# Performance work log

Measured on AMD Instinct MI355X. Metric: run time of the kernel, lower is better.

The kernel has to match this reference:

```python
import jax, jax.numpy as jnp
from jax import lax
import numpy as np

STRIDE = 1
PADDING = 1
DILATION = 1


def setup_inputs() -> dict:
    key = jax.random.key(0)
    k1, k2, k3, k4 = jax.random.split(key, 4)
    B, Cin, Cout, H, W, K, G = 32, 256, 256, 56, 56, 3, 8
    x = jax.random.normal(k1, (B, Cin, H, W), dtype=jnp.float32)
    conv = jax.random.normal(k2, (Cout, Cin, K, K), dtype=jnp.float32)
    S = jax.random.normal(k3, (Cin, G), dtype=jnp.float32)
    T = jax.random.normal(k4, (Cout, G), dtype=jnp.float32)
    return {"x": x, "conv": conv, "S": S, "T": T}


def reference(x, conv, S, T):
    # Faithful to FLGC.forward (training path).
    Cin = S.shape[0]
    Cout = T.shape[0]
    s_hat = jax.nn.softmax(S, axis=1)            # [Cin, G]
    t_hat = jax.nn.softmax(T, axis=1)            # [Cout, G]
    s = jnp.argmax(s_hat, axis=1)                # group id per input channel
    t = jnp.argmax(t_hat, axis=1)                # group id per output filter
    # Input channel c is scaled by s_hat[c, s[c]] inside its group.
    x_sc = x * s_hat[jnp.arange(Cin), s][None, :, None, None]
    # Filter o uses weight conv[o,c] * t_hat[o, t[o]] only where s[c] == t[o];
    # masking weights to zero elsewhere makes one dense conv equal the per-group convs.
    gate = (s[None, :] == t[:, None]).astype(conv.dtype)          # [Cout, Cin]
    w = conv * t_hat[jnp.arange(Cout), t][:, None, None, None] * gate[:, :, None, None]
    out_full = lax.conv_general_dilated(
        x_sc, w,
        window_strides=(STRIDE, STRIDE),
        padding=[(PADDING, PADDING), (PADDING, PADDING)],
        rhs_dilation=(DILATION, DILATION),
    )  # [B, Cout, H', W'], channel o = group-conv output of filter o
    # Original concatenates group outputs (channels ordered by perm = stable sort of t),
    # then indexes that with perm again: final[:, j] = out_full[:, perm[perm[j]]].
    perm = jnp.argsort(t * Cout + jnp.arange(Cout))  # stable group-major order
    return out_full[:, perm[perm]]
```

## Files before the change

kernel.cpp:

```cpp
#include <hip/hip_runtime.h>

#define M_SI    0
#define M_SO    256
#define M_CLIST 512
#define M_FLIST 768
#define M_DEST  1024
#define M_CBASE 1280
#define M_FBASE 1288
#define M_CCNT  1296
#define M_FCNT  1304
#define M_WOFFE 1312
#define WPACK_BYTE_OFF 16384
#define XR_BYTE_OFF   (4u << 20)
#define SLOT_ELEMS    3444736ull
#define SLOT_BYTES    (SLOT_ELEMS * 2ull)

typedef short bf16x8 __attribute__((ext_vector_type(8)));
typedef float f32x4  __attribute__((ext_vector_type(4)));

__device__ __forceinline__ unsigned short f2bf(float f) {
    unsigned u = __float_as_uint(f);
    u += 0x7fffu + ((u >> 16) & 1u);
    return (unsigned short)(u >> 16);
}

__device__ __forceinline__ void gl_lds16(const void* g, void* l) {
    __builtin_amdgcn_global_load_lds((const __attribute__((address_space(1))) unsigned int*)g,
                                     (__attribute__((address_space(3))) unsigned int*)l, 16, 0, 0);
}

__global__ __launch_bounds__(256) void flgc_setup(const float* __restrict__ S,
                                                  const float* __restrict__ T,
                                                  int* __restrict__ meta) {
    __shared__ float si[256], so[256];
    __shared__ int gin[256], gout[256];
    __shared__ int cnt_in[8], cnt_out[8], cb[8], fb[8];
    __shared__ int perm[256], destl[256];
    const int c = threadIdx.x;

    {
        float m = S[c * 8]; int am = 0;
        for (int k = 1; k < 8; ++k) { float v = S[c * 8 + k]; if (v > m) { m = v; am = k; } }
        float s = 0.f;
        for (int k = 0; k < 8; ++k) s += expf(S[c * 8 + k] - m);
        si[c] = 1.0f / s; gin[c] = am;
    }
    {
        float m = T[c * 8]; int am = 0;
        for (int k = 1; k < 8; ++k) { float v = T[c * 8 + k]; if (v > m) { m = v; am = k; } }
        float s = 0.f;
        for (int k = 0; k < 8; ++k) s += expf(T[c * 8 + k] - m);
        so[c] = 1.0f / s; gout[c] = am;
    }
    __syncthreads();
    const int g = gin[c], go = gout[c];
    int r1 = 0, r2 = 0;
    for (int i = 0; i < c; ++i) { r1 += (gin[i] == g); r2 += (gout[i] == go); }
    if (c < 8) {
        int n1 = 0, n2 = 0;
        for (int i = 0; i < 256; ++i) { n1 += (gin[i] == c); n2 += (gout[i] == c); }
        cnt_in[c] = n1; cnt_out[c] = n2;
    }
    __syncthreads();
    if (c == 0) {
        int a = 0, b = 0;
        for (int k = 0; k < 8; ++k) { cb[k] = a; a += cnt_in[k]; fb[k] = b; b += cnt_out[k]; }
    }
    __syncthreads();
    meta[M_CLIST + cb[g] + r1] = c;
    perm[fb[go] + r2] = c;
    __syncthreads();
    const int ppc = perm[perm[c]];
    destl[ppc] = c;
    __syncthreads();
    ((float*)meta)[M_SI + c] = si[c];
    ((float*)meta)[M_SO + c] = so[c];
    meta[M_FLIST + c] = perm[c];
    meta[M_DEST + c]  = destl[c];
    if (c < 8) {
        meta[M_CBASE + c] = cb[c];
        meta[M_FBASE + c] = fb[c];
        meta[M_CCNT + c]  = cnt_in[c];
        meta[M_FCNT + c]  = cnt_out[c];
    }
    if (c == 0) {
        int a = 0;
        for (int k = 0; k < 8; ++k) {
            meta[M_WOFFE + k] = a;
            const int nq  = (cnt_in[k] + 31) >> 5;
            const int mfa = (cnt_out[k] + 15) >> 4;
            a += nq * mfa * 9 * 512;
        }
        meta[M_WOFFE + 8] = a;
    }
}

__global__ void flgc_pack(const float* __restrict__ conv, const int* __restrict__ meta,
                          unsigned short* __restrict__ wpack) {
    const float* si = (const float*)meta + M_SI;
    const float* so = (const float*)meta + M_SO;
    const int total = meta[M_WOFFE + 8];
    for (int idx = blockIdx.x * blockDim.x + threadIdx.x; idx < total;
         idx += gridDim.x * blockDim.x) {
        int gg = 0;
        while (gg < 7 && idx >= meta[M_WOFFE + gg + 1]) ++gg;
        const int local = idx - meta[M_WOFFE + gg];
        const int fcnt = meta[M_FCNT + gg], ccnt = meta[M_CCNT + gg];
        const int mfall = (fcnt + 15) >> 4;
        const int fragidx = local >> 9, e = local & 511;
        const int lane = e >> 3, j = e & 7;
        const int tap = fragidx % 9, t2 = fragidx / 9;
        const int mf = t2 % mfall, q = t2 / mfall;
        const int fl = mf * 16 + (lane & 15);
        const int cl = q * 32 + (lane >> 4) * 8 + j;
        float v = 0.f;
        if (fl < fcnt && cl < ccnt) {
            const int F  = meta[M_FLIST + meta[M_FBASE + gg] + fl];
            const int CH = meta[M_CLIST + meta[M_CBASE + gg] + cl];
            v = conv[(F * 256 + CH) * 9 + tap] * si[CH] * so[F];
        }
        wpack[idx] = f2bf(v);
    }
}

__global__ __launch_bounds__(256) void flgc_reorder(const float* __restrict__ x,
                                                    const int* __restrict__ meta,
                                                    unsigned short* __restrict__ xr) {
    __shared__ float lds[32][65];
    const int r = blockIdx.x;
    const int b = blockIdx.y;
    const int slot = blockIdx.z;
    const int g = slot >> 1, q = slot & 1;
    const int ccnt = meta[M_CCNT + g];
    int nq = (ccnt + 31) >> 5; if (nq > 2) nq = 2;
    if (q >= nq) return;
    const int cbas = meta[M_CBASE + g];
    const int row = r - 1;
    const int colx = threadIdx.x & 63;
    const int cl0 = threadIdx.x >> 6;
    const int ic = colx - 1;
    const bool ok = ((unsigned)row < 56u) && ((unsigned)ic < 56u);

    int chn[8];
#pragma unroll
    for (int i = 0; i < 8; ++i) {
        const int cgl = q * 32 + cl0 + i * 4;
        chn[i] = (cgl < ccnt) ? meta[M_CLIST + cbas + cgl] : -1;
    }
    const float* xb = x + (size_t)b * 256 * 3136 + row * 56 + ic;
    float v[8];
#pragma unroll
    for (int i = 0; i < 8; ++i) v[i] = 0.f;
#pragma unroll
    for (int i = 0; i < 8; ++i)
        if (ok && chn[i] >= 0) v[i] = xb[(size_t)chn[i] * 3136];
#pragma unroll
    for (int i = 0; i < 8; ++i) lds[cl0 + i * 4][colx] = v[i];
    __syncthreads();

    unsigned short* dst = xr + (size_t)(slot * 32 + b) * 107648ull + r * 58 * 32;
    for (int i = threadIdx.x; i < 58 * 8; i += 256) {
        const int col = i >> 3, cl4 = (i & 7) * 4;
        ushort4 pk = make_ushort4(f2bf(lds[cl4 + 0][col]), f2bf(lds[cl4 + 1][col]),
                                  f2bf(lds[cl4 + 2][col]), f2bf(lds[cl4 + 3][col]));
        *(ushort4*)&dst[col * 32 + cl4] = pk;
    }
}

__global__ __launch_bounds__(256, 2) void flgc_conv_f(const int* __restrict__ meta,
                                                      const unsigned short* __restrict__ wpack,
                                                      const unsigned short* __restrict__ xr,
                                                      float* __restrict__ out) {
    __shared__ __align__(16) unsigned short xbuf[18944];
    __shared__ __align__(16) unsigned short wbuf[13824];
    const int g = blockIdx.z, b = blockIdx.y, h0 = blockIdx.x * 8;
    const int tid = threadIdx.x, lane = tid & 63, wv = tid >> 6;
    const int ccnt = meta[M_CCNT + g], fcnt = meta[M_FCNT + g];
    const int fbas = meta[M_FBASE + g];
    const int woffe = meta[M_WOFFE + g];
    int nq = (ccnt + 31) >> 5; if (nq > 2) nq = 2;
    const int mfall = (fcnt + 15) >> 4;
    if (mfall == 0) return;
    const int n = lane & 15, kg = lane >> 4;
    const int prow = 2 * wv + (n >> 3), pcol = n & 7;

    for (int mf0 = 0; mf0 < mfall; mf0 += 3) {
        const int mfe = min(3, mfall - mf0);
        f32x4 acc[3][7];
#pragma unroll
        for (int mf = 0; mf < 3; ++mf)
#pragma unroll
            for (int cg = 0; cg < 7; ++cg) acc[mf][cg] = (f32x4){0.f, 0.f, 0.f, 0.f};

        for (int q = 0; q < nq; ++q) {
            __syncthreads();
            const char* tbase = (const char*)(xr + (size_t)((g * 2 + q) * 32 + b) * 107648ull
                                              + (size_t)h0 * 58 * 32);
            for (int k = wv; k < 37; k += 4)
                gl_lds16(tbase + k * 1024 + lane * 16, (char*)xbuf + k * 1024);
            const char* wsrc = (const char*)(wpack + woffe + (size_t)(q * mfall + mf0) * 9 * 512);
            for (int k = wv; k < mfe * 9; k += 4)
                gl_lds16(wsrc + k * 1024 + lane * 16, (char*)wbuf + k * 1024);
            __syncthreads();
#pragma unroll
            for (int tap = 0; tap < 9; ++tap) {
                const int dr = tap / 3, dc = tap - dr * 3;
                bf16x8 A[3];
#pragma unroll
                for (int mf = 0; mf < 3; ++mf)
                    if (mf < mfe)
                        A[mf] = *(bf16x8*)&wbuf[(mf * 9 + tap) * 512 + lane * 8];
                const int rb = (prow + dr) * 58;
#pragma unroll
                for (int cg = 0; cg < 7; ++cg) {
                    const int colx = pcol + cg * 8 + dc;
                    const bf16x8 B = *(bf16x8*)&xbuf[(rb + colx) * 32 + kg * 8];
#pragma unroll
                    for (int mf = 0; mf < 3; ++mf)
                        if (mf < mfe)
                            acc[mf][cg] = __builtin_amdgcn_mfma_f32_16x16x32_bf16(
                                A[mf], B, acc[mf][cg], 0, 0, 0);
                }
            }
        }
#pragma unroll
        for (int mf = 0; mf < 3; ++mf) {
            if (mf < mfe) {
#pragma unroll
                for (int reg = 0; reg < 4; ++reg) {
                    const int fl = (mf0 + mf) * 16 + (lane >> 4) * 4 + reg;
                    if (fl < fcnt) {
                        const int F  = meta[M_FLIST + fbas + fl];
                        const int oc = meta[M_DEST + F];
                        float* op = out + ((size_t)(b * 256 + oc) * 56 + (h0 + prow)) * 56 + pcol;
#pragma unroll
                        for (int cg = 0; cg < 7; ++cg)
                            op[cg * 8] = acc[mf][cg][reg];
                    }
                }
            }
        }
    }
}

__global__ __launch_bounds__(256, 2) void flgc_conv_mfma(const float* __restrict__ x,
                                                         const int* __restrict__ meta,
                                                         const unsigned short* __restrict__ wpack,
                                                         float* __restrict__ out) {
    __shared__ __align__(16) unsigned short xlds[10 * 4 * 64 * 8];
    __shared__ __align__(16) unsigned short wlds[4 * 9 * 512];
    const int g = blockIdx.z, b = blockIdx.y, h0 = blockIdx.x * 8;
    const int tid = threadIdx.x, lane = tid & 63, wv = tid >> 6;
    const int ccnt = meta[M_CCNT + g], fcnt = meta[M_FCNT + g];
    const int cbas = meta[M_CBASE + g], fbas = meta[M_FBASE + g];
    const int woffe = meta[M_WOFFE + g];
    const int nq = (ccnt + 31) >> 5, mfall = (fcnt + 15) >> 4;
    if (mfall == 0) return;
    const int n = lane & 15, kgl = lane >> 4;
    const int prow = 2 * wv + (n >> 3);
    const int pcol = n & 7;

    for (int mf0 = 0; mf0 < mfall; mf0 += 4) {
        const int mfe = min(4, mfall - mf0);
        f32x4 acc[4][7];
#pragma unroll
        for (int mf = 0; mf < 4; ++mf)
#pragma unroll
            for (int cg = 0; cg < 7; ++cg) acc[mf][cg] = (f32x4){0.f, 0.f, 0.f, 0.f};

        for (int q = 0; q < nq; ++q) {
            __syncthreads();
            for (int widx = wv; widx < mfe * 9; widx += 4) {
                const int mf = widx / 9, tap = widx - mf * 9;
                const unsigned short* src =
                    wpack + woffe + (((q * mfall) + mf0 + mf) * 9 + tap) * 512 + lane * 8;
                *(bf16x8*)&wlds[(mf * 9 + tap) * 512 + lane * 8] = *(const bf16x8*)src;
            }
            for (int i = tid; i < 80 * 64; i += 256) {
                const int colx = i & 63, t = i >> 6;
                const int rr = t >> 3, cq = t & 7;
                const int c0 = q * 32 + cq * 4;
                const int row = h0 + rr - 1, ic = colx - 1;
                float v0 = 0.f, v1 = 0.f, v2 = 0.f, v3 = 0.f;
                if ((unsigned)row < 56u && (unsigned)ic < 56u) {
                    const float* xp = x + (size_t)(b * 256) * 3136 + row * 56 + ic;
                    if (c0 + 0 < ccnt) v0 = xp[(size_t)meta[M_CLIST + cbas + c0 + 0] * 3136];
                    if (c0 + 1 < ccnt) v1 = xp[(size_t)meta[M_CLIST + cbas + c0 + 1] * 3136];
                    if (c0 + 2 < ccnt) v2 = xp[(size_t)meta[M_CLIST + cbas + c0 + 2] * 3136];
                    if (c0 + 3 < ccnt) v3 = xp[(size_t)meta[M_CLIST + cbas + c0 + 3] * 3136];
                }
                ushort4 pk = make_ushort4(f2bf(v0), f2bf(v1), f2bf(v2), f2bf(v3));
                *(ushort4*)&xlds[(((rr * 4 + (cq >> 1)) * 64 + colx) << 3) + ((cq & 1) << 2)] = pk;
            }
            __syncthreads();
#pragma unroll
            for (int tap = 0; tap < 9; ++tap) {
                const int dr = tap / 3, dcp = tap - dr * 3;
                bf16x8 A[4];
#pragma unroll
                for (int mf = 0; mf < 4; ++mf)
                    if (mf < mfe)
                        A[mf] = *(bf16x8*)&wlds[(mf * 9 + tap) * 512 + lane * 8];
                const int row_r = prow + dr;
                const int xbase = ((row_r * 4 + kgl) * 64) << 3;
#pragma unroll
                for (int cg = 0; cg < 7; ++cg) {
                    const int cc = cg * 8 + pcol + dcp;
                    const bf16x8 B = *(bf16x8*)&xlds[xbase + (cc << 3)];
#pragma unroll
                    for (int mf = 0; mf < 4; ++mf)
                        if (mf < mfe)
                            acc[mf][cg] = __builtin_amdgcn_mfma_f32_16x16x32_bf16(
                                A[mf], B, acc[mf][cg], 0, 0, 0);
                }
            }
        }
#pragma unroll
        for (int mf = 0; mf < 4; ++mf) {
            if (mf < mfe) {
#pragma unroll
                for (int reg = 0; reg < 4; ++reg) {
                    const int fl = (mf0 + mf) * 16 + (lane >> 4) * 4 + reg;
                    if (fl < fcnt) {
                        const int F  = meta[M_FLIST + fbas + fl];
                        const int oc = meta[M_DEST + F];
                        float* op = out + ((size_t)(b * 256 + oc) * 56 + (h0 + prow)) * 56 + pcol;
#pragma unroll
                        for (int cg = 0; cg < 7; ++cg)
                            op[cg * 8] = acc[mf][cg][reg];
                    }
                }
            }
        }
    }
}

extern "C" void kernel_launch(void* const* d_in, const int* in_sizes, int n_in,
                              void* d_out, int out_size, void* d_ws, size_t ws_size,
                              hipStream_t stream) {
    const float* x    = (const float*)d_in[0];
    const float* conv = (const float*)d_in[1];
    const float* S    = (const float*)d_in[2];
    const float* T    = (const float*)d_in[3];
    float* out = (float*)d_out;
    int* meta = (int*)d_ws;
    unsigned short* wpack = (unsigned short*)((char*)d_ws + WPACK_BYTE_OFF);
    unsigned short* xr    = (unsigned short*)((char*)d_ws + XR_BYTE_OFF);

    flgc_setup<<<1, 256, 0, stream>>>(S, T, meta);
    flgc_pack<<<256, 256, 0, stream>>>(conv, meta, wpack);

    const size_t need = (size_t)XR_BYTE_OFF + 16ull * SLOT_BYTES + 4096;
    if (ws_size >= need) {
        flgc_reorder<<<dim3(58, 32, 16), 256, 0, stream>>>(x, meta, xr);
        flgc_conv_f<<<dim3(7, 32, 8), 256, 0, stream>>>(meta, wpack, xr, out);
    } else {
        flgc_conv_mfma<<<dim3(7, 32, 8), 256, 0, stream>>>(x, meta, wpack, out);
    }
}
```

Baseline: 116.0 us.

## Pipeline conv over row strips with double-buffered LDS and swizzled layout

Replaces the per-strip conv kernel with a persistent-per-(batch,group) kernel that walks all 7 row strips and both channel quarters, double-buffering the input tiles via async global-to-LDS loads so the next strip loads while the current one computes. The reorder kernel now XOR-swizzles 8-channel chunks to reduce LDS bank conflicts on the B-operand reads. Weights for up to 4 filter tiles are loaded once and kept resident, and output channel mappings are hoisted. In exchange the grid shrinks from 1792 to 256 blocks at one block per CU, which risks under-filling the GPU and adds register pressure from the larger accumulator set.

```diff
diff --git a/kernel.cpp b/kernel.cpp
--- a/kernel.cpp
+++ b/kernel.cpp
@@ -14,6 +14,7 @@
 #define XR_BYTE_OFF   (4u << 20)
 #define SLOT_ELEMS    3444736ull
 #define SLOT_BYTES    (SLOT_ELEMS * 2ull)
+#define CHX 40
 
 typedef short bf16x8 __attribute__((ext_vector_type(8)));
 typedef float f32x4  __attribute__((ext_vector_type(4)));
@@ -160,85 +161,136 @@
 
     unsigned short* dst = xr + (size_t)(slot * 32 + b) * 107648ull + r * 58 * 32;
     for (int i = threadIdx.x; i < 58 * 8; i += 256) {
-        const int col = i >> 3, cl4 = (i & 7) * 4;
+        const int col = i >> 3, c8 = i & 7;
+        const int chunk = c8 >> 1, lo = (c8 & 1) * 4;
+        const int cl4 = chunk * 8 + lo;
         ushort4 pk = make_ushort4(f2bf(lds[cl4 + 0][col]), f2bf(lds[cl4 + 1][col]),
                                   f2bf(lds[cl4 + 2][col]), f2bf(lds[cl4 + 3][col]));
-        *(ushort4*)&dst[col * 32 + cl4] = pk;
-    }
-}
-
-__global__ __launch_bounds__(256, 2) void flgc_conv_f(const int* __restrict__ meta,
+        const int schunk = chunk ^ ((col >> 1) & 3);
+        *(ushort4*)&dst[col * 32 + schunk * 8 + lo] = pk;
+    }
+}
+
+__global__ __launch_bounds__(256, 1) void flgc_conv_p(const int* __restrict__ meta,
                                                       const unsigned short* __restrict__ wpack,
                                                       const unsigned short* __restrict__ xr,
                                                       float* __restrict__ out) {
-    __shared__ __align__(16) unsigned short xbuf[18944];
-    __shared__ __align__(16) unsigned short wbuf[13824];
-    const int g = blockIdx.z, b = blockIdx.y, h0 = blockIdx.x * 8;
+    __shared__ __align__(16) unsigned short xbuf[2][CHX * 512];
+    __shared__ __align__(16) unsigned short wbuf[2 * 4 * 9 * 512];
+    const int b = blockIdx.x, g = blockIdx.y;
     const int tid = threadIdx.x, lane = tid & 63, wv = tid >> 6;
     const int ccnt = meta[M_CCNT + g], fcnt = meta[M_FCNT + g];
-    const int fbas = meta[M_FBASE + g];
-    const int woffe = meta[M_WOFFE + g];
+    const int fbas = meta[M_FBASE + g], woffe = meta[M_WOFFE + g];
     int nq = (ccnt + 31) >> 5; if (nq > 2) nq = 2;
     const int mfall = (fcnt + 15) >> 4;
     if (mfall == 0) return;
     const int n = lane & 15, kg = lane >> 4;
     const int prow = 2 * wv + (n >> 3), pcol = n & 7;
-
-    for (int mf0 = 0; mf0 < mfall; mf0 += 3) {
-        const int mfe = min(3, mfall - mf0);
-        f32x4 acc[3][7];
-#pragma unroll
-        for (int mf = 0; mf < 3; ++mf)
-#pragma unroll
-            for (int cg = 0; cg < 7; ++cg) acc[mf][cg] = (f32x4){0.f, 0.f, 0.f, 0.f};
-
-        for (int q = 0; q < nq; ++q) {
-            __syncthreads();
-            const char* tbase = (const char*)(xr + (size_t)((g * 2 + q) * 32 + b) * 107648ull
-                                              + (size_t)h0 * 58 * 32);
-            for (int k = wv; k < 37; k += 4)
-                gl_lds16(tbase + k * 1024 + lane * 16, (char*)xbuf + k * 1024);
-            const char* wsrc = (const char*)(wpack + woffe + (size_t)(q * mfall + mf0) * 9 * 512);
-            for (int k = wv; k < mfe * 9; k += 4)
-                gl_lds16(wsrc + k * 1024 + lane * 16, (char*)wbuf + k * 1024);
-            __syncthreads();
+    const size_t slotbase = ((size_t)(g * 2) * 32 + b) * 107648ull;
+    const size_t qstride = 32ull * 107648ull;
+
+    for (int mf0 = 0; mf0 < mfall; mf0 += 4) {
+        const int mfe = min(4, mfall - mf0);
+        int ocv[4][4];
+#pragma unroll
+        for (int mf = 0; mf < 4; ++mf)
+#pragma unroll
+            for (int reg = 0; reg < 4; ++reg) {
+                const int fl = (mf0 + mf) * 16 + (lane >> 4) * 4 + reg;
+                int oc = -1;
+                if (mf < mfe && fl < fcnt)
+                    oc = meta[M_DEST + meta[M_FLIST + fbas + fl]];
+                ocv[mf][reg] = oc;
+            }
+        if (nq == 0) {
+            for (int s = 0; s < 7; ++s) {
+                const int h = s * 8 + prow;
+#pragma unroll
+                for (int mf = 0; mf < 4; ++mf)
+#pragma unroll
+                    for (int reg = 0; reg < 4; ++reg)
+                        if (ocv[mf][reg] >= 0) {
+                            float* op = out + ((size_t)(b * 256 + ocv[mf][reg]) * 56 + h) * 56 + pcol;
+#pragma unroll
+                            for (int cg = 0; cg < 7; ++cg) op[cg * 8] = 0.f;
+                        }
+            }
+            continue;
+        }
+        __syncthreads();
+        const int wch = nq * mfe * 9;
+        for (int k = wv; k < wch; k += 4) {
+            const int q = k / (mfe * 9), r = k - q * mfe * 9;
+            const int mf = r / 9, tap = r - mf * 9;
+            const unsigned short* src =
+                wpack + woffe + ((size_t)(q * mfall + mf0 + mf) * 9 + tap) * 512 + lane * 8;
+            gl_lds16(src, &wbuf[((q * 4 + mf) * 9 + tap) * 512 + lane * 8]);
+        }
+        __syncthreads();
+
+        const int P = 7 * nq;
+        for (int k = wv; k < CHX; k += 4)
+            gl_lds16((const char*)(xr + slotbase) + k * 1024 + lane * 16,
+                     (char*)&xbuf[0][0] + k * 1024);
+        f32x4 acc[4][7];
+        for (int p = 0; p < P; ++p) {
+            const int s = p / nq, q = p - s * nq;
+            if (p + 1 < P) {
+                const int s2 = (p + 1) / nq, q2 = (p + 1) - s2 * nq;
+                const size_t base = slotbase + (size_t)q2 * qstride + (size_t)s2 * 14848;
+                for (int k = wv; k < CHX; k += 4)
+                    gl_lds16((const char*)(xr + base) + k * 1024 + lane * 16,
+                             (char*)&xbuf[(p + 1) & 1][0] + k * 1024);
+                asm volatile("s_waitcnt vmcnt(10)" ::: "memory");
+            } else {
+                asm volatile("s_waitcnt vmcnt(0)" ::: "memory");
+            }
+            __builtin_amdgcn_s_barrier();
+            __builtin_amdgcn_sched_barrier(0);
+            const unsigned short* xb = &xbuf[p & 1][0];
+            if (q == 0) {
+#pragma unroll
+                for (int mf = 0; mf < 4; ++mf)
+#pragma unroll
+                    for (int cg = 0; cg < 7; ++cg) acc[mf][cg] = (f32x4){0.f, 0.f, 0.f, 0.f};
+            }
 #pragma unroll
             for (int tap = 0; tap < 9; ++tap) {
                 const int dr = tap / 3, dc = tap - dr * 3;
-                bf16x8 A[3];
-#pragma unroll
-                for (int mf = 0; mf < 3; ++mf)
+                bf16x8 A[4];
+#pragma unroll
+                for (int mf = 0; mf < 4; ++mf)
                     if (mf < mfe)
-                        A[mf] = *(bf16x8*)&wbuf[(mf * 9 + tap) * 512 + lane * 8];
+                        A[mf] = *(const bf16x8*)&wbuf[((q * 4 + mf) * 9 + tap) * 512 + lane * 8];
                 const int rb = (prow + dr) * 58;
 #pragma unroll
                 for (int cg = 0; cg < 7; ++cg) {
                     const int colx = pcol + cg * 8 + dc;
-                    const bf16x8 B = *(bf16x8*)&xbuf[(rb + colx) * 32 + kg * 8];
-#pragma unroll
-                    for (int mf = 0; mf < 3; ++mf)
+                    const bf16x8 B = *(const bf16x8*)
+                        &xb[(rb + colx) * 32 + ((kg ^ ((colx >> 1) & 3)) << 3)];
+#pragma unroll
+                    for (int mf = 0; mf < 4; ++mf)
                         if (mf < mfe)
                             acc[mf][cg] = __builtin_amdgcn_mfma_f32_16x16x32_bf16(
                                 A[mf], B, acc[mf][cg], 0, 0, 0);
                 }
             }
-        }
-#pragma unroll
-        for (int mf = 0; mf < 3; ++mf) {
-            if (mf < mfe) {
-#pragma unroll
-                for (int reg = 0; reg < 4; ++reg) {
-                    const int fl = (mf0 + mf) * 16 + (lane >> 4) * 4 + reg;
-                    if (fl < fcnt) {
-                        const int F  = meta[M_FLIST + fbas + fl];
-                        const int oc = meta[M_DEST + F];
-                        float* op = out + ((size_t)(b * 256 + oc) * 56 + (h0 + prow)) * 56 + pcol;
-#pragma unroll
-                        for (int cg = 0; cg < 7; ++cg)
-                            op[cg * 8] = acc[mf][cg][reg];
+            if (q == nq - 1) {
+                const int h = s * 8 + prow;
+#pragma unroll
+                for (int mf = 0; mf < 4; ++mf)
+#pragma unroll
+                    for (int reg = 0; reg < 4; ++reg) {
+                        const int oc = ocv[mf][reg];
+                        if (oc >= 0) {
+                            float* op = out + ((size_t)(b * 256 + oc) * 56 + h) * 56 + pcol;
+#pragma unroll
+                            for (int cg = 0; cg < 7; ++cg) op[cg * 8] = acc[mf][cg][reg];
+                        }
                     }
-                }
-            }
+            }
+            __builtin_amdgcn_sched_barrier(0);
+            __builtin_amdgcn_s_barrier();
         }
     }
 }
@@ -350,10 +402,10 @@
     flgc_setup<<<1, 256, 0, stream>>>(S, T, meta);
     flgc_pack<<<256, 256, 0, stream>>>(conv, meta, wpack);
 
-    const size_t need = (size_t)XR_BYTE_OFF + 16ull * SLOT_BYTES + 4096;
+    const size_t need = (size_t)XR_BYTE_OFF + 16ull * SLOT_BYTES + 65536;
     if (ws_size >= need) {
         flgc_reorder<<<dim3(58, 32, 16), 256, 0, stream>>>(x, meta, xr);
-        flgc_conv_f<<<dim3(7, 32, 8), 256, 0, stream>>>(meta, wpack, xr, out);
+        flgc_conv_p<<<dim3(32, 8), 256, 0, stream>>>(meta, wpack, xr, out);
     } else {
         flgc_conv_mfma<<<dim3(7, 32, 8), 256, 0, stream>>>(x, meta, wpack, out);
     }
```

Measured after the change: 157.1 us. 1.35x slower.
